# Optimization experiments

Hardware: AMD Instinct MI355X
Metric: run time of the kernel (lower is better)

Reference implementation:

```python
import jax, jax.numpy as jnp
import numpy as np

B, T, C = 2, 2048, 2048
N_HEAD = 16
HEAD_DIM = C // N_HEAD


def setup_inputs() -> dict:
    key = jax.random.key(0)
    ks = jax.random.split(key, 5)
    s = 1.0 / np.sqrt(C)
    return {
        "x": jax.random.normal(ks[0], (B, T, C), dtype=jnp.float32),
        "Wq": jax.random.normal(ks[1], (C, C), dtype=jnp.float32) * s,
        "bq": jnp.zeros((C,), dtype=jnp.float32),
        "Wk": jax.random.normal(ks[2], (C, C), dtype=jnp.float32) * s,
        "bk": jnp.zeros((C,), dtype=jnp.float32),
        "Wv": jax.random.normal(ks[3], (C, C), dtype=jnp.float32) * s,
        "bv": jnp.zeros((C,), dtype=jnp.float32),
        "Wp": jax.random.normal(ks[4], (C, C), dtype=jnp.float32) * s,
        "bp": jnp.zeros((C,), dtype=jnp.float32),
    }


def reference(x, Wq, bq, Wk, bk, Wv, bv, Wp, bp):
    Bx, Tx, Cx = x.shape
    # torch nn.Linear: y = x @ W.T + b
    def lin(x, W, b):
        return jnp.einsum("btc,dc->btd", x, W) + b

    def split_heads(y):  # (B,T,C) -> (B,H,T,hd)
        return y.reshape(Bx, Tx, N_HEAD, HEAD_DIM).transpose(0, 2, 1, 3)

    q = split_heads(lin(x, Wq, bq))
    k = split_heads(lin(x, Wk, bk))
    v = split_heads(lin(x, Wv, bv))

    scale = 1.0 / np.sqrt(HEAD_DIM).astype(np.float32)
    attn = jnp.einsum("bhqd,bhkd->bhqk", q, k) * scale  # (B,H,T,T)
    causal = jnp.tril(jnp.ones((Tx, Tx), dtype=bool))
    attn = jnp.where(causal[None, None], attn, -jnp.inf)
    attn = jax.nn.softmax(attn, axis=-1)
    out = jnp.einsum("bhqk,bhkd->bhqd", attn, v)  # (B,H,T,hd)
    # Faithful to original: transpose(-2,-1) swaps T and head_dim, then
    # a contiguous view reinterprets memory as (B,T,C).
    out = out.transpose(0, 1, 3, 2).reshape(Bx, Tx, Cx)
    return lin(out, Wp, bp)
```

## Files before the change

### kernel.cpp

```cpp
#include <hip/hip_runtime.h>
#include <stdint.h>

#define DEVI __device__ __forceinline__

typedef __attribute__((ext_vector_type(8))) short short8;
typedef __attribute__((ext_vector_type(4))) float f32x4;
typedef __attribute__((ext_vector_type(4))) unsigned int u32x4;

static constexpr int Bn = 2;
static constexpr int Tn = 2048;
static constexpr int Cn = 2048;
static constexpr int NH = 16;
static constexpr int HD = 128;
static constexpr int Kdim = 2048;

DEVI unsigned short f2bf(float f) {
  union { float f; unsigned u; } v; v.f = f;
  return (unsigned short)((v.u + 0x7FFFu + ((v.u >> 16) & 1u)) >> 16);
}

DEVI void gload_lds16(const void* g, void* l) {
  __builtin_amdgcn_global_load_lds(
      (const __attribute__((address_space(1))) void*)g,
      (__attribute__((address_space(3))) void*)l, 16, 0, 0);
}

__global__ __launch_bounds__(256) void cast_bf16_kernel(
    const float* __restrict__ src, unsigned short* __restrict__ dst, int n) {
  int idx = (blockIdx.x * blockDim.x + threadIdx.x) * 4;
  const int stride = gridDim.x * blockDim.x * 4;
  for (; idx < n; idx += stride) {
    f32x4 f = *(const f32x4*)(src + idx);
    unsigned short o[4];
    o[0] = f2bf(f[0]); o[1] = f2bf(f[1]); o[2] = f2bf(f[2]); o[3] = f2bf(f[3]);
    *(unsigned long long*)(dst + idx) = *(const unsigned long long*)o;
  }
}

__global__ __launch_bounds__(256) void cast4_kernel(
    const float* __restrict__ s0, const float* __restrict__ s1,
    const float* __restrict__ s2, const float* __restrict__ s3,
    unsigned short* __restrict__ d0, unsigned short* __restrict__ d1,
    unsigned short* __restrict__ d2, unsigned short* __restrict__ d3, int n) {
  const int w = blockIdx.y;
  const float* src = (w == 0) ? s0 : (w == 1) ? s1 : (w == 2) ? s2 : s3;
  unsigned short* dst = (w == 0) ? d0 : (w == 1) ? d1 : (w == 2) ? d2 : d3;
  int idx = (blockIdx.x * blockDim.x + threadIdx.x) * 4;
  const int stride = gridDim.x * blockDim.x * 4;
  for (; idx < n; idx += stride) {
    f32x4 f = *(const f32x4*)(src + idx);
    unsigned short o[4];
    o[0] = f2bf(f[0]); o[1] = f2bf(f[1]); o[2] = f2bf(f[2]); o[3] = f2bf(f[3]);
    *(unsigned long long*)(dst + idx) = *(const unsigned long long*)o;
  }
}

__global__ __launch_bounds__(256) void gemm_qkv_fused_kernel(
    const unsigned short* __restrict__ X,
    const unsigned short* __restrict__ Wq_, const unsigned short* __restrict__ Wk_,
    const unsigned short* __restrict__ Wv_,
    const float* __restrict__ bq_, const float* __restrict__ bk_, const float* __restrict__ bv_,
    unsigned short* __restrict__ Qo, unsigned short* __restrict__ Ko,
    unsigned short* __restrict__ Vo) {
  __shared__ unsigned short As[128 * 32];
  __shared__ unsigned short Bs[128 * 32];
  const int tid = threadIdx.x;
  const int wave = tid >> 6, lane = tid & 63;
  const int wm = wave >> 1, wn = wave & 1;
  const int quad = lane >> 4, lr = lane & 15;

  const int nidx = blockIdx.x;
  const int m0 = blockIdx.y * 128;
  const int sel = nidx >> 4;
  const int n0 = (nidx & 15) * 128;
  const unsigned short* W = (sel == 0) ? Wq_ : (sel == 1) ? Wk_ : Wv_;
  const float* bias = (sel == 0) ? bq_ : (sel == 1) ? bk_ : bv_;

  f32x4 acc[4][4];
  const f32x4 zero4 = {0.f, 0.f, 0.f, 0.f};
#pragma unroll
  for (int i = 0; i < 4; ++i)
#pragma unroll
    for (int j = 0; j < 4; ++j) acc[i][j] = zero4;

  const int srow = tid >> 2;
  const int scol = (((tid & 3) ^ ((srow >> 1) & 3)) * 8);
  const unsigned short* Ag = X + (size_t)(m0 + srow) * Kdim + scol;
  const unsigned short* Bg = W + (size_t)(n0 + srow) * Kdim + scol;
  unsigned short* Al = &As[tid * 8];
  unsigned short* Bl = &Bs[tid * 8];
  const int fsw = (quad ^ ((lr >> 1) & 3)) * 8;

  for (int k0 = 0; k0 < Kdim; k0 += 32) {
    gload_lds16(Ag + k0, Al);
    gload_lds16(Ag + (size_t)64 * Kdim + k0, Al + 2048);
    gload_lds16(Bg + k0, Bl);
    gload_lds16(Bg + (size_t)64 * Kdim + k0, Bl + 2048);
    __syncthreads();
    short8 af[4], bf[4];
#pragma unroll
    for (int mi = 0; mi < 4; ++mi)
      af[mi] = *(const short8*)&As[(wm * 64 + mi * 16 + lr) * 32 + fsw];
#pragma unroll
    for (int ni = 0; ni < 4; ++ni)
      bf[ni] = *(const short8*)&Bs[(wn * 64 + ni * 16 + lr) * 32 + fsw];
#pragma unroll
    for (int mi = 0; mi < 4; ++mi)
#pragma unroll
      for (int ni = 0; ni < 4; ++ni)
        acc[mi][ni] = __builtin_amdgcn_mfma_f32_16x16x32_bf16(af[mi], bf[ni], acc[mi][ni], 0, 0, 0);
    __syncthreads();
  }

  if (sel == 2) {
#pragma unroll
    for (int ni = 0; ni < 4; ++ni) {
      const int n = n0 + wn * 64 + ni * 16 + lr;
      const float bv = bias[n];
      const int h = n >> 7, d = n & 127;
#pragma unroll
      for (int mi = 0; mi < 4; ++mi) {
        const int m = m0 + wm * 64 + mi * 16 + quad * 4;
        const int b = m >> 11, t = m & 2047;
        unsigned short o4[4];
#pragma unroll
        for (int r = 0; r < 4; ++r) o4[r] = f2bf(acc[mi][ni][r] + bv);
        *(unsigned long long*)&Vo[(((size_t)(b * NH + h)) * HD + d) * Tn + t] =
            *(const unsigned long long*)o4;
      }
    }
  } else {
    unsigned short* Out = (sel == 0) ? Qo : Ko;
#pragma unroll
    for (int ni = 0; ni < 4; ++ni) {
      const int n = n0 + wn * 64 + ni * 16 + lr;
      const float bv = bias[n];
      const int h = n >> 7, d = n & 127;
#pragma unroll
      for (int mi = 0; mi < 4; ++mi) {
#pragma unroll
        for (int r = 0; r < 4; ++r) {
          const int m = m0 + wm * 64 + mi * 16 + quad * 4 + r;
          const int b = m >> 11, t = m & 2047;
          Out[(((size_t)(b * NH + h)) * Tn + t) * HD + d] = f2bf(acc[mi][ni][r] + bv);
        }
      }
    }
  }
}

__global__ __launch_bounds__(256) void gemm_proj_kernel(
    const unsigned short* __restrict__ Aall,
    const unsigned short* __restrict__ W,
    const float* __restrict__ bias,
    float* __restrict__ Y) {
  __shared__ unsigned short As[128 * 32];
  __shared__ unsigned short Bs[128 * 32];
  const int tid = threadIdx.x;
  const int wave = tid >> 6, lane = tid & 63;
  const int wm = wave >> 1, wn = wave & 1;
  const int quad = lane >> 4, lr = lane & 15;

  const int m0 = blockIdx.y * 128, n0 = blockIdx.x * 128;
  const int bz = blockIdx.z;
  const unsigned short* A = Aall + (size_t)bz * Cn * Tn;

  f32x4 acc[4][4];
  const f32x4 zero4 = {0.f, 0.f, 0.f, 0.f};
#pragma unroll
  for (int i = 0; i < 4; ++i)
#pragma unroll
    for (int j = 0; j < 4; ++j) acc[i][j] = zero4;

  const int srow = tid >> 2;
  const int scol = (((tid & 3) ^ ((srow >> 1) & 3)) * 8);
  const unsigned short* Ag = A + (size_t)(m0 + srow) * Kdim + scol;
  const unsigned short* Bg = W + (size_t)(n0 + srow) * Kdim + scol;
  unsigned short* Al = &As[tid * 8];
  unsigned short* Bl = &Bs[tid * 8];
  const int fsw = (quad ^ ((lr >> 1) & 3)) * 8;

  for (int k0 = 0; k0 < Kdim; k0 += 32) {
    gload_lds16(Ag + k0, Al);
    gload_lds16(Ag + (size_t)64 * Kdim + k0, Al + 2048);
    gload_lds16(Bg + k0, Bl);
    gload_lds16(Bg + (size_t)64 * Kdim + k0, Bl + 2048);
    __syncthreads();
    short8 af[4], bf[4];
#pragma unroll
    for (int mi = 0; mi < 4; ++mi)
      af[mi] = *(const short8*)&As[(wm * 64 + mi * 16 + lr) * 32 + fsw];
#pragma unroll
    for (int ni = 0; ni < 4; ++ni)
      bf[ni] = *(const short8*)&Bs[(wn * 64 + ni * 16 + lr) * 32 + fsw];
#pragma unroll
    for (int mi = 0; mi < 4; ++mi)
#pragma unroll
      for (int ni = 0; ni < 4; ++ni)
        acc[mi][ni] = __builtin_amdgcn_mfma_f32_16x16x32_bf16(af[mi], bf[ni], acc[mi][ni], 0, 0, 0);
    __syncthreads();
  }

#pragma unroll
  for (int ni = 0; ni < 4; ++ni) {
    const int n = n0 + wn * 64 + ni * 16 + lr;
    const float bv = bias[n];
#pragma unroll
    for (int mi = 0; mi < 4; ++mi) {
#pragma unroll
      for (int r = 0; r < 4; ++r) {
        const int m = m0 + wm * 64 + mi * 16 + quad * 4 + r;
        Y[((size_t)bz * Tn + m) * Cn + n] = acc[mi][ni][r] + bv;
      }
    }
  }
}

__global__ __launch_bounds__(256, 1) void attn_kernel(
    const unsigned short* __restrict__ Q,
    const unsigned short* __restrict__ K,
    const unsigned short* __restrict__ V,
    unsigned short* __restrict__ Ot) {
  constexpr int KST = 136;
  constexpr int VST = 136;
  constexpr int PST = 136;
  __shared__ unsigned short Ks[128 * KST];
  __shared__ unsigned short Vs[144 * VST];
  __shared__ unsigned short Ps[128 * PST];

  const int tid = threadIdx.x;
  const int wave = tid >> 6, lane = tid & 63;
  const int quad = lane >> 4, lr = lane & 15;
  const int bh = blockIdx.y;
  const float SL = 0.08838834764831845f * 1.4426950408889634f;

  const unsigned short* Kp = K + (size_t)bh * Tn * HD;
  const unsigned short* Vp = V + (size_t)bh * HD * Tn;
  unsigned short* Pw = &Ps[wave * 32 * PST];

  for (int i = tid; i < 16 * VST; i += 256) Vs[128 * VST + i] = 0x3F80;

  const f32x4 zero4 = {0.f, 0.f, 0.f, 0.f};
#pragma unroll 1
  for (int half = 0; half < 2; ++half) {
    const int jt = half ? (15 - (int)blockIdx.x) : (int)blockIdx.x;
    const int q0 = jt * 128;

    const unsigned short* Qp = Q + ((size_t)bh * Tn + q0 + wave * 32) * HD;
    short8 qf[2][4];
#pragma unroll
    for (int mi = 0; mi < 2; ++mi)
#pragma unroll
      for (int ks = 0; ks < 4; ++ks)
        qf[mi][ks] = *(const short8*)&Qp[(mi * 16 + lr) * HD + ks * 32 + quad * 8];

    f32x4 oacc[2][9];
#pragma unroll
    for (int mi = 0; mi < 2; ++mi)
#pragma unroll
      for (int nd = 0; nd < 9; ++nd) oacc[mi][nd] = zero4;

    const int nch = q0 / 128 + 1;
    for (int c = 0; c < nch; ++c) {
      const int k0 = c * 128;
      {
        const int r = tid >> 1;
        const int cc = (tid & 1) * 64;
        const unsigned short* kg = &Kp[(size_t)(k0 + r) * HD + cc];
        const unsigned short* vg = &Vp[(size_t)r * Tn + k0 + cc];
        unsigned short* kl = &Ks[r * KST + cc];
        unsigned short* vl = &Vs[r * VST + cc];
#pragma unroll
        for (int p = 0; p < 8; ++p) {
          *(u32x4*)(kl + p * 8) = *(const u32x4*)(kg + p * 8);
          *(u32x4*)(vl + p * 8) = *(const u32x4*)(vg + p * 8);
        }
      }
      __syncthreads();

      f32x4 sa[2][8];
#pragma unroll
      for (int mi = 0; mi < 2; ++mi)
#pragma unroll
        for (int nt = 0; nt < 8; ++nt) sa[mi][nt] = zero4;
#pragma unroll
      for (int nt = 0; nt < 8; ++nt) {
        short8 kf[4];
#pragma unroll
        for (int ks = 0; ks < 4; ++ks)
          kf[ks] = *(const short8*)&Ks[(nt * 16 + lr) * KST + ks * 32 + quad * 8];
#pragma unroll
        for (int mi = 0; mi < 2; ++mi)
#pragma unroll
          for (int ks = 0; ks < 4; ++ks)
            sa[mi][nt] = __builtin_amdgcn_mfma_f32_16x16x32_bf16(qf[mi][ks], kf[ks], sa[mi][nt], 0, 0, 0);
      }

      if (k0 == q0) {
#pragma unroll
        for (int mi = 0; mi < 2; ++mi)
#pragma unroll
          for (int nt = 0; nt < 8; ++nt)
#pragma unroll
            for (int r = 0; r < 4; ++r) {
              const int qg = q0 + wave * 32 + mi * 16 + quad * 4 + r;
              const int kg = k0 + nt * 16 + lr;
              if (kg > qg) sa[mi][nt][r] = -3.0e38f;
            }
      }

#pragma unroll
      for (int mi = 0; mi < 2; ++mi)
#pragma unroll
        for (int nt = 0; nt < 8; ++nt)
#pragma unroll
          for (int r = 0; r < 4; ++r) {
            const float p = __builtin_amdgcn_exp2f(sa[mi][nt][r] * SL);
            Pw[(mi * 16 + quad * 4 + r) * PST + nt * 16 + lr] = f2bf(p);
          }

#pragma unroll
      for (int kt = 0; kt < 4; ++kt) {
        short8 pf[2];
#pragma unroll
        for (int mi = 0; mi < 2; ++mi)
          pf[mi] = *(const short8*)&Pw[(mi * 16 + lr) * PST + kt * 32 + quad * 8];
#pragma unroll
        for (int nd = 0; nd < 9; ++nd) {
          short8 vf = *(const short8*)&Vs[(nd * 16 + lr) * VST + kt * 32 + quad * 8];
#pragma unroll
          for (int mi = 0; mi < 2; ++mi)
            oacc[mi][nd] = __builtin_amdgcn_mfma_f32_16x16x32_bf16(pf[mi], vf, oacc[mi][nd], 0, 0, 0);
        }
      }
      __syncthreads();
    }

#pragma unroll
    for (int mi = 0; mi < 2; ++mi)
#pragma unroll
      for (int r = 0; r < 4; ++r) {
        const float rl = 1.0f / oacc[mi][8][r];
        const int tl = wave * 32 + mi * 16 + quad * 4 + r;
#pragma unroll
        for (int nd = 0; nd < 8; ++nd)
          Ps[tl * PST + nd * 16 + lr] = f2bf(oacc[mi][nd][r] * rl);
      }
    __syncthreads();
    {
      unsigned short* Od = Ot + (size_t)bh * HD * Tn + q0;
#pragma unroll
      for (int p = 0; p < 8; ++p) {
        const int d = p * 16 + (tid >> 4);
        const int t8 = (tid & 15) * 8;
        alignas(16) unsigned short v[8];
#pragma unroll
        for (int j = 0; j < 8; ++j) v[j] = Ps[(t8 + j) * PST + d];
        *(u32x4*)&Od[(size_t)d * Tn + t8] = *(const u32x4*)v;
      }
    }
    __syncthreads();
  }
}

extern "C" void kernel_launch(void* const* d_in, const int* in_sizes, int n_in,
                              void* d_out, int out_size, void* d_ws, size_t ws_size,
                              hipStream_t stream) {
  const float* x  = (const float*)d_in[0];
  const float* Wq = (const float*)d_in[1];
  const float* bq = (const float*)d_in[2];
  const float* Wk = (const float*)d_in[3];
  const float* bk = (const float*)d_in[4];
  const float* Wv = (const float*)d_in[5];
  const float* bv = (const float*)d_in[6];
  const float* Wp = (const float*)d_in[7];
  const float* bp = (const float*)d_in[8];
  float* out = (float*)d_out;

  char* ws = (char*)d_ws;
  const size_t MB = 1ull << 20;
  unsigned short* Xbf = (unsigned short*)(ws);
  unsigned short* Wqb = (unsigned short*)(ws + 16 * MB);
  unsigned short* Wkb = (unsigned short*)(ws + 24 * MB);
  unsigned short* Wvb = (unsigned short*)(ws + 32 * MB);
  unsigned short* Wpb = (unsigned short*)(ws + 40 * MB);
  unsigned short* Qb  = (unsigned short*)(ws + 48 * MB);
  unsigned short* Kb  = (unsigned short*)(ws + 64 * MB);
  unsigned short* Vtb = (unsigned short*)(ws + 80 * MB);
  unsigned short* Otb = (unsigned short*)(ws + 96 * MB);

  cast_bf16_kernel<<<dim3(1024), dim3(256), 0, stream>>>(x, Xbf, Bn * Tn * Cn);
  cast4_kernel<<<dim3(512, 4), dim3(256), 0, stream>>>(
      Wq, Wk, Wv, Wp, Wqb, Wkb, Wvb, Wpb, Cn * Cn);

  gemm_qkv_fused_kernel<<<dim3(48, 32), dim3(256), 0, stream>>>(
      Xbf, Wqb, Wkb, Wvb, bq, bk, bv, Qb, Kb, Vtb);

  attn_kernel<<<dim3(8, Bn * NH), dim3(256), 0, stream>>>(Qb, Kb, Vtb, Otb);

  gemm_proj_kernel<<<dim3(16, 16, 2), dim3(256), 0, stream>>>(Otb, Wpb, bp, out);
}
```

Before: 444.2 us.

## Share K/V tiles across paired query blocks and merge cast kernels

The attention kernel now processes both paired query tiles (j and 15-j) in one pass over the key chunks, so each K/V chunk is loaded once and used by both tiles instead of being reloaded per half. K/V loads go straight to LDS through global_load_lds with an XOR-swizzled layout that replaces the padded strides. The S tile is computed transposed so P can be packed and written as 64-bit stores with truncating bf16 conversion. The x cast and the weight casts are merged into a single launch. This doubles the live accumulator and Q-fragment registers, which risks spills at one block per CU.

```diff
diff --git a/kernel.cpp b/kernel.cpp
--- a/kernel.cpp
+++ b/kernel.cpp
@@ -25,26 +25,17 @@
       (__attribute__((address_space(3))) void*)l, 16, 0, 0);
 }
 
-__global__ __launch_bounds__(256) void cast_bf16_kernel(
-    const float* __restrict__ src, unsigned short* __restrict__ dst, int n) {
-  int idx = (blockIdx.x * blockDim.x + threadIdx.x) * 4;
-  const int stride = gridDim.x * blockDim.x * 4;
-  for (; idx < n; idx += stride) {
-    f32x4 f = *(const f32x4*)(src + idx);
-    unsigned short o[4];
-    o[0] = f2bf(f[0]); o[1] = f2bf(f[1]); o[2] = f2bf(f[2]); o[3] = f2bf(f[3]);
-    *(unsigned long long*)(dst + idx) = *(const unsigned long long*)o;
-  }
-}
-
-__global__ __launch_bounds__(256) void cast4_kernel(
+__global__ __launch_bounds__(256) void cast5_kernel(
     const float* __restrict__ s0, const float* __restrict__ s1,
     const float* __restrict__ s2, const float* __restrict__ s3,
+    const float* __restrict__ s4,
     unsigned short* __restrict__ d0, unsigned short* __restrict__ d1,
-    unsigned short* __restrict__ d2, unsigned short* __restrict__ d3, int n) {
+    unsigned short* __restrict__ d2, unsigned short* __restrict__ d3,
+    unsigned short* __restrict__ d4, int n0, int nw) {
   const int w = blockIdx.y;
-  const float* src = (w == 0) ? s0 : (w == 1) ? s1 : (w == 2) ? s2 : s3;
-  unsigned short* dst = (w == 0) ? d0 : (w == 1) ? d1 : (w == 2) ? d2 : d3;
+  const float* src = (w == 0) ? s0 : (w == 1) ? s1 : (w == 2) ? s2 : (w == 3) ? s3 : s4;
+  unsigned short* dst = (w == 0) ? d0 : (w == 1) ? d1 : (w == 2) ? d2 : (w == 3) ? d3 : d4;
+  const int n = (w == 0) ? n0 : nw;
   int idx = (blockIdx.x * blockDim.x + threadIdx.x) * 4;
   const int stride = gridDim.x * blockDim.x * 4;
   for (; idx < n; idx += stride) {
@@ -216,135 +207,148 @@
   }
 }
 
+constexpr int PST = 136;
+DEVI void attn_tile_chunk(
+    const unsigned short* Ks, const unsigned short* Vs, unsigned short* Pw,
+    const short8 qf[2][4], f32x4 (*oacc)[9], int q0w, int k0, bool diag,
+    int quad, int lr) {
+  const float SL = 0.08838834764831845f * 1.4426950408889634f;
+  const f32x4 zero4 = {0.f, 0.f, 0.f, 0.f};
+#pragma unroll
+  for (int np = 0; np < 4; ++np) {
+    short8 kf[2][4];
+#pragma unroll
+    for (int j = 0; j < 2; ++j)
+#pragma unroll
+      for (int ks = 0; ks < 4; ++ks)
+        kf[j][ks] = *(const short8*)&Ks[((np * 2 + j) * 16 + lr) * 128 +
+                                        (((ks * 4 + quad) ^ lr) * 8)];
+    f32x4 s[2][2];
+#pragma unroll
+    for (int j = 0; j < 2; ++j)
+#pragma unroll
+      for (int mi = 0; mi < 2; ++mi) s[j][mi] = zero4;
+#pragma unroll
+    for (int ks = 0; ks < 4; ++ks)
+#pragma unroll
+      for (int j = 0; j < 2; ++j)
+#pragma unroll
+        for (int mi = 0; mi < 2; ++mi)
+          s[j][mi] = __builtin_amdgcn_mfma_f32_16x16x32_bf16(kf[j][ks], qf[mi][ks], s[j][mi], 0, 0, 0);
+#pragma unroll
+    for (int j = 0; j < 2; ++j)
+#pragma unroll
+      for (int mi = 0; mi < 2; ++mi) {
+        const int nt = np * 2 + j;
+        if (diag) {
+          const int q = q0w + mi * 16 + lr;
+#pragma unroll
+          for (int r = 0; r < 4; ++r) {
+            const int key = k0 + nt * 16 + quad * 4 + r;
+            if (key > q) s[j][mi][r] = -3.0e38f;
+          }
+        }
+        union { float f; unsigned u; } a0, a1, a2, a3;
+        a0.f = __builtin_amdgcn_exp2f(s[j][mi][0] * SL);
+        a1.f = __builtin_amdgcn_exp2f(s[j][mi][1] * SL);
+        a2.f = __builtin_amdgcn_exp2f(s[j][mi][2] * SL);
+        a3.f = __builtin_amdgcn_exp2f(s[j][mi][3] * SL);
+        const unsigned lo = (a0.u >> 16) | (a1.u & 0xffff0000u);
+        const unsigned hi = (a2.u >> 16) | (a3.u & 0xffff0000u);
+        const unsigned long long pv = (unsigned long long)lo | ((unsigned long long)hi << 32);
+        *(unsigned long long*)&Pw[(mi * 16 + lr) * PST + nt * 16 + quad * 4] = pv;
+      }
+  }
+#pragma unroll
+  for (int kt = 0; kt < 4; ++kt) {
+    short8 pf[2];
+#pragma unroll
+    for (int mi = 0; mi < 2; ++mi)
+      pf[mi] = *(const short8*)&Pw[(mi * 16 + lr) * PST + kt * 32 + quad * 8];
+#pragma unroll
+    for (int nd = 0; nd < 9; ++nd) {
+      short8 vf = *(const short8*)&Vs[(nd * 16 + lr) * 128 + (((kt * 4 + quad) ^ lr) * 8)];
+#pragma unroll
+      for (int mi = 0; mi < 2; ++mi)
+        oacc[mi][nd] = __builtin_amdgcn_mfma_f32_16x16x32_bf16(pf[mi], vf, oacc[mi][nd], 0, 0, 0);
+    }
+  }
+}
+
 __global__ __launch_bounds__(256, 1) void attn_kernel(
     const unsigned short* __restrict__ Q,
     const unsigned short* __restrict__ K,
     const unsigned short* __restrict__ V,
     unsigned short* __restrict__ Ot) {
-  constexpr int KST = 136;
-  constexpr int VST = 136;
-  constexpr int PST = 136;
-  __shared__ unsigned short Ks[128 * KST];
-  __shared__ unsigned short Vs[144 * VST];
+  __shared__ unsigned short Ks[128 * 128];
+  __shared__ unsigned short Vs[144 * 128];
   __shared__ unsigned short Ps[128 * PST];
 
   const int tid = threadIdx.x;
   const int wave = tid >> 6, lane = tid & 63;
   const int quad = lane >> 4, lr = lane & 15;
   const int bh = blockIdx.y;
-  const float SL = 0.08838834764831845f * 1.4426950408889634f;
+
+  const int jA = blockIdx.x, jB = 15 - jA;
+  const int q0A = jA * 128, q0B = jB * 128;
 
   const unsigned short* Kp = K + (size_t)bh * Tn * HD;
   const unsigned short* Vp = V + (size_t)bh * HD * Tn;
   unsigned short* Pw = &Ps[wave * 32 * PST];
 
-  for (int i = tid; i < 16 * VST; i += 256) Vs[128 * VST + i] = 0x3F80;
-
+  for (int i = tid; i < 16 * 128; i += 256) Vs[128 * 128 + i] = 0x3F80;
+
+  short8 qfA[2][4], qfB[2][4];
+  {
+    const unsigned short* QpA = Q + ((size_t)bh * Tn + q0A + wave * 32) * HD;
+    const unsigned short* QpB = Q + ((size_t)bh * Tn + q0B + wave * 32) * HD;
+#pragma unroll
+    for (int mi = 0; mi < 2; ++mi)
+#pragma unroll
+      for (int ks = 0; ks < 4; ++ks) {
+        qfA[mi][ks] = *(const short8*)&QpA[(mi * 16 + lr) * HD + ks * 32 + quad * 8];
+        qfB[mi][ks] = *(const short8*)&QpB[(mi * 16 + lr) * HD + ks * 32 + quad * 8];
+      }
+  }
+
+  f32x4 oaccA[2][9], oaccB[2][9];
   const f32x4 zero4 = {0.f, 0.f, 0.f, 0.f};
+#pragma unroll
+  for (int mi = 0; mi < 2; ++mi)
+#pragma unroll
+    for (int nd = 0; nd < 9; ++nd) { oaccA[mi][nd] = zero4; oaccB[mi][nd] = zero4; }
+
+  const int rl = lane >> 4, ch = lane & 15;
+
+  for (int c = 0; c <= jB; ++c) {
+    const int k0 = c * 128;
+#pragma unroll
+    for (int i = 0; i < 8; ++i) {
+      const int row = wave * 32 + i * 4 + rl;
+      const int g = (ch ^ (row & 15)) * 8;
+      gload_lds16(Kp + (size_t)(k0 + row) * HD + g, &Ks[row * 128 + ch * 8]);
+      gload_lds16(Vp + (size_t)row * Tn + k0 + g, &Vs[row * 128 + ch * 8]);
+    }
+    __syncthreads();
+    attn_tile_chunk(Ks, Vs, Pw, qfB, oaccB, q0B + wave * 32, k0, c == jB, quad, lr);
+    if (c <= jA)
+      attn_tile_chunk(Ks, Vs, Pw, qfA, oaccA, q0A + wave * 32, k0, c == jA, quad, lr);
+    __syncthreads();
+  }
+
 #pragma unroll 1
-  for (int half = 0; half < 2; ++half) {
-    const int jt = half ? (15 - (int)blockIdx.x) : (int)blockIdx.x;
-    const int q0 = jt * 128;
-
-    const unsigned short* Qp = Q + ((size_t)bh * Tn + q0 + wave * 32) * HD;
-    short8 qf[2][4];
+  for (int e = 0; e < 2; ++e) {
+    const f32x4 (*oacc)[9] = e ? (const f32x4(*)[9])oaccA : (const f32x4(*)[9])oaccB;
+    const int q0 = e ? q0A : q0B;
 #pragma unroll
     for (int mi = 0; mi < 2; ++mi)
 #pragma unroll
-      for (int ks = 0; ks < 4; ++ks)
-        qf[mi][ks] = *(const short8*)&Qp[(mi * 16 + lr) * HD + ks * 32 + quad * 8];
-
-    f32x4 oacc[2][9];
-#pragma unroll
-    for (int mi = 0; mi < 2; ++mi)
-#pragma unroll
-      for (int nd = 0; nd < 9; ++nd) oacc[mi][nd] = zero4;
-
-    const int nch = q0 / 128 + 1;
-    for (int c = 0; c < nch; ++c) {
-      const int k0 = c * 128;
-      {
-        const int r = tid >> 1;
-        const int cc = (tid & 1) * 64;
-        const unsigned short* kg = &Kp[(size_t)(k0 + r) * HD + cc];
-        const unsigned short* vg = &Vp[(size_t)r * Tn + k0 + cc];
-        unsigned short* kl = &Ks[r * KST + cc];
-        unsigned short* vl = &Vs[r * VST + cc];
-#pragma unroll
-        for (int p = 0; p < 8; ++p) {
-          *(u32x4*)(kl + p * 8) = *(const u32x4*)(kg + p * 8);
-          *(u32x4*)(vl + p * 8) = *(const u32x4*)(vg + p * 8);
-        }
-      }
-      __syncthreads();
-
-      f32x4 sa[2][8];
-#pragma unroll
-      for (int mi = 0; mi < 2; ++mi)
-#pragma unroll
-        for (int nt = 0; nt < 8; ++nt) sa[mi][nt] = zero4;
-#pragma unroll
-      for (int nt = 0; nt < 8; ++nt) {
-        short8 kf[4];
-#pragma unroll
-        for (int ks = 0; ks < 4; ++ks)
-          kf[ks] = *(const short8*)&Ks[(nt * 16 + lr) * KST + ks * 32 + quad * 8];
-#pragma unroll
-        for (int mi = 0; mi < 2; ++mi)
-#pragma unroll
-          for (int ks = 0; ks < 4; ++ks)
-            sa[mi][nt] = __builtin_amdgcn_mfma_f32_16x16x32_bf16(qf[mi][ks], kf[ks], sa[mi][nt], 0, 0, 0);
-      }
-
-      if (k0 == q0) {
-#pragma unroll
-        for (int mi = 0; mi < 2; ++mi)
-#pragma unroll
-          for (int nt = 0; nt < 8; ++nt)
-#pragma unroll
-            for (int r = 0; r < 4; ++r) {
-              const int qg = q0 + wave * 32 + mi * 16 + quad * 4 + r;
-              const int kg = k0 + nt * 16 + lr;
-              if (kg > qg) sa[mi][nt][r] = -3.0e38f;
-            }
-      }
-
-#pragma unroll
-      for (int mi = 0; mi < 2; ++mi)
-#pragma unroll
-        for (int nt = 0; nt < 8; ++nt)
-#pragma unroll
-          for (int r = 0; r < 4; ++r) {
-            const float p = __builtin_amdgcn_exp2f(sa[mi][nt][r] * SL);
-            Pw[(mi * 16 + quad * 4 + r) * PST + nt * 16 + lr] = f2bf(p);
-          }
-
-#pragma unroll
-      for (int kt = 0; kt < 4; ++kt) {
-        short8 pf[2];
-#pragma unroll
-        for (int mi = 0; mi < 2; ++mi)
-          pf[mi] = *(const short8*)&Pw[(mi * 16 + lr) * PST + kt * 32 + quad * 8];
-#pragma unroll
-        for (int nd = 0; nd < 9; ++nd) {
-          short8 vf = *(const short8*)&Vs[(nd * 16 + lr) * VST + kt * 32 + quad * 8];
-#pragma unroll
-          for (int mi = 0; mi < 2; ++mi)
-            oacc[mi][nd] = __builtin_amdgcn_mfma_f32_16x16x32_bf16(pf[mi], vf, oacc[mi][nd], 0, 0, 0);
-        }
-      }
-      __syncthreads();
-    }
-
-#pragma unroll
-    for (int mi = 0; mi < 2; ++mi)
-#pragma unroll
       for (int r = 0; r < 4; ++r) {
-        const float rl = 1.0f / oacc[mi][8][r];
+        const float rlv = 1.0f / oacc[mi][8][r];
         const int tl = wave * 32 + mi * 16 + quad * 4 + r;
 #pragma unroll
         for (int nd = 0; nd < 8; ++nd)
-          Ps[tl * PST + nd * 16 + lr] = f2bf(oacc[mi][nd][r] * rl);
+          Ps[tl * PST + nd * 16 + lr] = f2bf(oacc[mi][nd][r] * rlv);
       }
     __syncthreads();
     {
@@ -389,9 +393,8 @@
   unsigned short* Vtb = (unsigned short*)(ws + 80 * MB);
   unsigned short* Otb = (unsigned short*)(ws + 96 * MB);
 
-  cast_bf16_kernel<<<dim3(1024), dim3(256), 0, stream>>>(x, Xbf, Bn * Tn * Cn);
-  cast4_kernel<<<dim3(512, 4), dim3(256), 0, stream>>>(
-      Wq, Wk, Wv, Wp, Wqb, Wkb, Wvb, Wpb, Cn * Cn);
+  cast5_kernel<<<dim3(512, 5), dim3(256), 0, stream>>>(
+      x, Wq, Wk, Wv, Wp, Xbf, Wqb, Wkb, Wvb, Wpb, Bn * Tn * Cn, Cn * Cn);
 
   gemm_qkv_fused_kernel<<<dim3(48, 32), dim3(256), 0, stream>>>(
       Xbf, Wqb, Wkb, Wvb, bq, bk, bv, Qb, Kb, Vtb);
```

Measured after the change: 522.2 us. 1.18x slower.
